# Performance work log

Measured on AMD Instinct MI355X. Metric: run time of the kernel, lower is better.

## Reference

```python
import jax, jax.numpy as jnp
import numpy as np

N_HEAD = 8
LN_EPS = 1e-5


def _ln(x, g, b):
    m = jnp.mean(x, axis=-1, keepdims=True)
    v = jnp.mean((x - m) ** 2, axis=-1, keepdims=True)
    return (x - m) * jax.lax.rsqrt(v + LN_EPS) * g + b


def setup_inputs() -> dict:
    B, S, IN, D, F, OUT, L = 4, 2048, 3, 512, 2048, 20, 6
    key = jax.random.key(0)
    ks = jax.random.split(key, 22)
    sc = 0.02
    return {
        'src': jax.random.normal(ks[0], (B, S, IN), jnp.float32),
        'W_in': jax.random.normal(ks[1], (IN, D), jnp.float32) * sc,
        'b_in': jnp.zeros((D,), jnp.float32),
        'Wq': jax.random.normal(ks[2], (L, D, D), jnp.float32) * sc,
        'bq': jnp.zeros((L, D), jnp.float32),
        'Wk': jax.random.normal(ks[3], (L, D, D), jnp.float32) * sc,
        'bk': jnp.zeros((L, D), jnp.float32),
        'Wv': jax.random.normal(ks[4], (L, D, D), jnp.float32) * sc,
        'bv': jnp.zeros((L, D), jnp.float32),
        'Wo': jax.random.normal(ks[5], (L, D, D), jnp.float32) * sc,
        'bo': jnp.zeros((L, D), jnp.float32),
        'ln1_g': jnp.ones((L, D), jnp.float32),
        'ln1_b': jnp.zeros((L, D), jnp.float32),
        'W1': jax.random.normal(ks[6], (L, D, F), jnp.float32) * sc,
        'b1': jnp.zeros((L, F), jnp.float32),
        'W2': jax.random.normal(ks[7], (L, F, D), jnp.float32) * sc,
        'b2': jnp.zeros((L, D), jnp.float32),
        'ln2_g': jnp.ones((L, D), jnp.float32),
        'ln2_b': jnp.zeros((L, D), jnp.float32),
        'W_out': jax.random.normal(ks[8], (D, OUT), jnp.float32) * sc,
        'b_out': jnp.zeros((OUT,), jnp.float32),
    }


def reference(src, W_in, b_in, Wq, bq, Wk, bk, Wv, bv, Wo, bo, ln1_g, ln1_b,
              W1, b1, W2, b2, ln2_g, ln2_b, W_out, b_out):
    x = src @ W_in + b_in            # [B, S, D]
    B, S, D = x.shape
    dh = D // N_HEAD
    scale = 1.0 / np.sqrt(dh).astype(np.float32)

    def layer(x, p):
        wq, biq, wk, bik, wv, biv, wo, bio, g1, be1, w1, bi1, w2, bi2, g2, be2 = p
        q = (x @ wq + biq).reshape(B, S, N_HEAD, dh)
        k = (x @ wk + bik).reshape(B, S, N_HEAD, dh)
        v = (x @ wv + biv).reshape(B, S, N_HEAD, dh)
        # flex_attention with score_mod=None == plain scaled dot-product attention
        scores = jnp.einsum('bqhd,bkhd->bhqk', q, k) * scale
        a = jax.nn.softmax(scores, axis=-1)
        o = jnp.einsum('bhqk,bkhd->bqhd', a, v).reshape(B, S, D)
        attn = o @ wo + bio
        h = _ln(x + attn, g1, be1)                       # post-norm (norm_first=False)
        ff = jax.nn.relu(h @ w1 + bi1) @ w2 + bi2
        h = _ln(h + ff, g2, be2)
        return h, None

    x, _ = jax.lax.scan(layer, x, (Wq, bq, Wk, bk, Wv, bv, Wo, bo,
                                   ln1_g, ln1_b, W1, b1, W2, b2, ln2_g, ln2_b))
    return x @ W_out + b_out         # [B, S, OUT]
```

## Files before the change

kernel.cpp:

```cpp
#include <hip/hip_runtime.h>

typedef unsigned short u16;
typedef unsigned int u32;
typedef __bf16 bf16x8 __attribute__((ext_vector_type(8)));
typedef float f32x4 __attribute__((ext_vector_type(4)));
typedef float f32x16 __attribute__((ext_vector_type(16)));

__device__ __forceinline__ u16 f2bf(float f) {
    union { float f; u32 u; } v; v.f = f;
    u32 r = v.u + 0x7FFFu + ((v.u >> 16) & 1u);
    return (u16)(r >> 16);
}

__device__ __forceinline__ u16 bfu(float x) {
    __bf16 b = (__bf16)x;
    union { __bf16 b; u16 u; } c; c.b = b; return c.u;
}

__device__ __forceinline__ void gload16(const u16* g, u16* l) {
    __builtin_amdgcn_global_load_lds((const __attribute__((address_space(1))) void*)g,
                                     (__attribute__((address_space(3))) void*)l, 16, 0, 0);
}

__global__ void wtrans(const float* __restrict__ W, u16* __restrict__ Wt,
                       int K, int N, int rowOff, int dstLd, long long dstStride)
{
    __shared__ float tile[32][33];
    const int l = blockIdx.z;
    const float* Wl = W + (size_t)l * K * N;
    u16* Wtl = Wt + (size_t)l * dstStride;
    const int tx = threadIdx.x, ty = threadIdx.y;
    const int x = blockIdx.x * 32 + tx;
    const int y0 = blockIdx.y * 32;
#pragma unroll
    for (int j = 0; j < 32; j += 8) tile[ty + j][tx] = Wl[(size_t)(y0 + ty + j) * N + x];
    __syncthreads();
    const int n0 = blockIdx.x * 32;
    const int k = y0 + tx;
#pragma unroll
    for (int j = 0; j < 32; j += 8)
        Wtl[(size_t)(rowOff + n0 + ty + j) * dstLd + k] = f2bf(tile[tx][ty + j]);
}

__global__ __launch_bounds__(256) void input_proj(const float* __restrict__ src,
    const float* __restrict__ Wi, const float* __restrict__ bi,
    float* __restrict__ xf, u16* __restrict__ xb)
{
    int idx = blockIdx.x * 256 + threadIdx.x;
    int m = idx >> 9, n = idx & 511;
    float v = bi[n] + src[m * 3] * Wi[n] + src[m * 3 + 1] * Wi[512 + n] + src[m * 3 + 2] * Wi[1024 + n];
    xf[idx] = v;
    xb[idx] = f2bf(v);
}

template<int EPI>
__global__ __launch_bounds__(256) void gemm_bt(
    const u16* __restrict__ A, const u16* __restrict__ Bt,
    const float* __restrict__ bias,
    float* __restrict__ Cf, u16* __restrict__ Cb,
    u16* __restrict__ Qo, u16* __restrict__ Ko, u16* __restrict__ Vo,
    const float* __restrict__ bq, const float* __restrict__ bk, const float* __restrict__ bv,
    int M, int N, int K)
{
    __shared__ u16 As[128 * 64];
    __shared__ u16 Bs[128 * 64];
    const int tid = threadIdx.x;
    const int lane = tid & 63, wid = tid >> 6;
    const int row0 = blockIdx.y * 128, col0 = blockIdx.x * 128;
    const int wr = (wid >> 1) * 64, wc = (wid & 1) * 64;
    const int cc = lane & 15, qg = lane >> 4;
    const int sr = tid >> 3, sg = tid & 7;
    f32x4 acc[4][4] = {};
    for (int k0 = 0; k0 < K; k0 += 64) {
        __syncthreads();
#pragma unroll
        for (int j = 0; j < 4; j++) {
            int r = j * 32 + sr;
            int gsw = (sg ^ (r & 7)) * 8;
            gload16(A + (size_t)(row0 + r) * K + k0 + gsw, &As[(j * 256 + tid) * 8]);
        }
#pragma unroll
        for (int j = 0; j < 4; j++) {
            int r = j * 32 + sr;
            int gsw = (sg ^ (r & 7)) * 8;
            gload16(Bt + (size_t)(col0 + r) * K + k0 + gsw, &Bs[(j * 256 + tid) * 8]);
        }
        __syncthreads();
        bf16x8 af[4][2], bfr[4][2];
#pragma unroll
        for (int i = 0; i < 4; i++) {
            int r = wr + i * 16 + cc;
#pragma unroll
            for (int kk = 0; kk < 2; kk++)
                af[i][kk] = *(const bf16x8*)&As[r * 64 + ((kk * 4 + qg) ^ (r & 7)) * 8];
        }
#pragma unroll
        for (int i = 0; i < 4; i++) {
            int r = wc + i * 16 + cc;
#pragma unroll
            for (int kk = 0; kk < 2; kk++)
                bfr[i][kk] = *(const bf16x8*)&Bs[r * 64 + ((kk * 4 + qg) ^ (r & 7)) * 8];
        }
#pragma unroll
        for (int mi = 0; mi < 4; mi++)
#pragma unroll
            for (int ni = 0; ni < 4; ni++) {
                acc[mi][ni] = __builtin_amdgcn_mfma_f32_16x16x32_bf16(af[mi][0], bfr[ni][0], acc[mi][ni], 0, 0, 0);
                acc[mi][ni] = __builtin_amdgcn_mfma_f32_16x16x32_bf16(af[mi][1], bfr[ni][1], acc[mi][ni], 0, 0, 0);
            }
    }
    const int q4 = qg * 4;
    if (EPI == 2) {
#pragma unroll
        for (int mi = 0; mi < 4; mi++) {
            int grow = row0 + wr + mi * 16 + q4;
            int btok = grow >> 11, srem = grow & 2047;
#pragma unroll
            for (int ni = 0; ni < 4; ni++) {
                int gcol = col0 + wc + ni * 16 + cc;
                int sec = gcol >> 9, f = gcol & 511;
                int hh = f >> 6, dd = f & 63;
                if (sec == 0) {
                    float bb = bq[f];
                    size_t base = (((size_t)btok * 8 + hh) * 2048 + srem) * 64 + dd;
#pragma unroll
                    for (int i = 0; i < 4; i++) Qo[base + (size_t)i * 64] = f2bf((acc[mi][ni][i] + bb) * 0.18033688f);
                } else if (sec == 1) {
                    float bb = bk[f];
                    size_t base = (((size_t)btok * 8 + hh) * 2048 + srem) * 64 + dd;
#pragma unroll
                    for (int i = 0; i < 4; i++) Ko[base + (size_t)i * 64] = f2bf(acc[mi][ni][i] + bb);
                } else {
                    float bb = bv[f];
                    size_t base = (((size_t)btok * 8 + hh) * 64 + dd) * 2048 + srem;
#pragma unroll
                    for (int i = 0; i < 4; i++) Vo[base + i] = f2bf(acc[mi][ni][i] + bb);
                }
            }
        }
    } else {
#pragma unroll
        for (int mi = 0; mi < 4; mi++) {
            int grow = row0 + wr + mi * 16 + q4;
#pragma unroll
            for (int ni = 0; ni < 4; ni++) {
                int gcol = col0 + wc + ni * 16 + cc;
                float bb = bias[gcol];
#pragma unroll
                for (int i = 0; i < 4; i++) {
                    float v = acc[mi][ni][i] + bb;
                    if (EPI == 0) Cf[(size_t)(grow + i) * N + gcol] = v;
                    else          Cb[(size_t)(grow + i) * N + gcol] = f2bf(v > 0.f ? v : 0.f);
                }
            }
        }
    }
}

__global__ __launch_bounds__(256) void gemm_bt_n64(
    const u16* __restrict__ A, const u16* __restrict__ Bt,
    const float* __restrict__ bias, float* __restrict__ Cf,
    int M, int N, int K)
{
    __shared__ u16 As[128 * 64];
    __shared__ u16 Bs[64 * 64];
    const int tid = threadIdx.x;
    const int lane = tid & 63, wid = tid >> 6;
    const int row0 = blockIdx.y * 128, col0 = blockIdx.x * 64;
    const int wr = (wid >> 1) * 64, wc = (wid & 1) * 32;
    const int cc = lane & 15, qg = lane >> 4;
    f32x4 acc[4][2] = {};
    for (int k0 = 0; k0 < K; k0 += 64) {
        __syncthreads();
#pragma unroll
        for (int j = 0; j < 4; j++) {
            int s = j * 256 + tid;
            int r = s >> 3, g = s & 7;
            gload16(A + (size_t)(row0 + r) * K + k0 + (g ^ (r & 7)) * 8, &As[s * 8]);
        }
#pragma unroll
        for (int j = 0; j < 2; j++) {
            int s = j * 256 + tid;
            int r = s >> 3, g = s & 7;
            gload16(Bt + (size_t)(col0 + r) * K + k0 + (g ^ (r & 7)) * 8, &Bs[s * 8]);
        }
        __syncthreads();
        bf16x8 af[4][2], bfr[2][2];
#pragma unroll
        for (int i = 0; i < 4; i++) {
            int r = wr + i * 16 + cc;
#pragma unroll
            for (int kk = 0; kk < 2; kk++) {
                int g = kk * 4 + qg;
                af[i][kk] = *(const bf16x8*)&As[r * 64 + (g ^ (r & 7)) * 8];
            }
        }
#pragma unroll
        for (int i = 0; i < 2; i++) {
            int r = wc + i * 16 + cc;
#pragma unroll
            for (int kk = 0; kk < 2; kk++) {
                int g = kk * 4 + qg;
                bfr[i][kk] = *(const bf16x8*)&Bs[r * 64 + (g ^ (r & 7)) * 8];
            }
        }
#pragma unroll
        for (int mi = 0; mi < 4; mi++)
#pragma unroll
            for (int ni = 0; ni < 2; ni++) {
                acc[mi][ni] = __builtin_amdgcn_mfma_f32_16x16x32_bf16(af[mi][0], bfr[ni][0], acc[mi][ni], 0, 0, 0);
                acc[mi][ni] = __builtin_amdgcn_mfma_f32_16x16x32_bf16(af[mi][1], bfr[ni][1], acc[mi][ni], 0, 0, 0);
            }
    }
    const int q4 = qg * 4;
#pragma unroll
    for (int mi = 0; mi < 4; mi++) {
        int grow = row0 + wr + mi * 16 + q4;
#pragma unroll
        for (int ni = 0; ni < 2; ni++) {
            int gcol = col0 + wc + ni * 16 + cc;
            float bb = bias[gcol];
#pragma unroll
            for (int i = 0; i < 4; i++)
                Cf[(size_t)(grow + i) * N + gcol] = acc[mi][ni][i] + bb;
        }
    }
}

__global__ __launch_bounds__(256) void flash_attn(
    const u16* __restrict__ Qb, const u16* __restrict__ Kb, const u16* __restrict__ Vt,
    u16* __restrict__ Ob)
{
    __shared__ u16 Ks[2][4096];
    __shared__ u16 Vs[2][4096];
    const int tid = threadIdx.x, lane = tid & 63, w = tid >> 6;
    const int l31 = lane & 31, h = lane >> 5;
    const int bh = blockIdx.x, qt = blockIdx.y;
    const u16* Kg = Kb + (size_t)bh * (2048 * 64);
    const u16* Vg = Vt + (size_t)bh * (64 * 2048);

    bf16x8 qf[4];
    {
        const u16* Qrow = Qb + ((size_t)bh * 2048 + (size_t)qt * 128 + w * 32 + l31) * 64;
#pragma unroll
        for (int f = 0; f < 4; f++) qf[f] = *(const bf16x8*)(Qrow + f * 16 + h * 8);
    }
    f32x16 os0{}, os1{};
    float lsum = 0.f;

    const int r8 = lane >> 3;
    const int cswz = ((lane & 7) ^ r8) * 8;
#pragma unroll
    for (int cc = 0; cc < 2; cc++) {
        int c = w * 2 + cc;
        gload16(Kg + (size_t)(c * 8 + r8) * 64 + cswz, &Ks[0][c * 512]);
        gload16(Vg + (size_t)(c * 8 + r8) * 2048 + cswz, &Vs[0][c * 512]);
    }
    const int swz = (l31 & 7) << 3;

    for (int kt = 0; kt < 32; kt++) {
        const int cur = kt & 1;
        asm volatile("s_waitcnt vmcnt(0)" ::: "memory");
        __syncthreads();
        if (kt < 31) {
#pragma unroll
            for (int cc = 0; cc < 2; cc++) {
                int c = w * 2 + cc;
                gload16(Kg + (size_t)(kt + 1) * 4096 + (size_t)(c * 8 + r8) * 64 + cswz, &Ks[cur ^ 1][c * 512]);
                gload16(Vg + (size_t)(c * 8 + r8) * 2048 + (size_t)(kt + 1) * 64 + cswz, &Vs[cur ^ 1][c * 512]);
            }
        }
        f32x16 p0{}, p1{};
        {
            const u16* kb = &Ks[cur][0];
            __builtin_amdgcn_s_setprio(1);
#pragma unroll
            for (int f = 0; f < 4; f++) {
                int colu = (f * 16 + h * 8) ^ swz;
                bf16x8 ka0 = *(const bf16x8*)(kb + l31 * 64 + colu);
                bf16x8 ka1 = *(const bf16x8*)(kb + (32 + l31) * 64 + colu);
                p0 = __builtin_amdgcn_mfma_f32_32x32x16_bf16(ka0, qf[f], p0, 0, 0, 0);
                p1 = __builtin_amdgcn_mfma_f32_32x32x16_bf16(ka1, qf[f], p1, 0, 0, 0);
            }
            __builtin_amdgcn_s_setprio(0);
        }
        float ss[4] = {};
#pragma unroll
        for (int r = 0; r < 16; r++) { float e = __builtin_amdgcn_exp2f(p0[r]); p0[r] = e; ss[r & 3] += e; }
#pragma unroll
        for (int r = 0; r < 16; r++) { float e = __builtin_amdgcn_exp2f(p1[r]); p1[r] = e; ss[r & 3] += e; }
        lsum += (ss[0] + ss[1]) + (ss[2] + ss[3]);
        const u16* vb = &Vs[cur][0];
#pragma unroll
        for (int t = 0; t < 2; t++) {
            u32 pk[8], sw[8];
#pragma unroll
            for (int j = 0; j < 8; j++) {
                float a = t ? p1[2 * j] : p0[2 * j];
                float b = t ? p1[2 * j + 1] : p0[2 * j + 1];
                pk[j] = (u32)bfu(a) | ((u32)bfu(b) << 16);
                sw[j] = __shfl_xor(pk[j], 32);
            }
            union { u32 u[4]; bf16x8 v; } fA, fB;
            fA.u[0] = h ? sw[2] : pk[0];
            fA.u[1] = h ? sw[3] : pk[1];
            fA.u[2] = h ? pk[2] : sw[0];
            fA.u[3] = h ? pk[3] : sw[1];
            fB.u[0] = h ? sw[6] : pk[4];
            fB.u[1] = h ? sw[7] : pk[5];
            fB.u[2] = h ? pk[6] : sw[4];
            fB.u[3] = h ? pk[7] : sw[5];
            __builtin_amdgcn_s_setprio(1);
#pragma unroll
            for (int f = 0; f < 2; f++) {
                bf16x8 pa = f ? fB.v : fA.v;
                int colu = (t * 32 + f * 16 + h * 8) ^ swz;
                bf16x8 v0 = *(const bf16x8*)(vb + l31 * 64 + colu);
                bf16x8 v1 = *(const bf16x8*)(vb + (32 + l31) * 64 + colu);
                os0 = __builtin_amdgcn_mfma_f32_32x32x16_bf16(pa, v0, os0, 0, 0, 0);
                os1 = __builtin_amdgcn_mfma_f32_32x32x16_bf16(pa, v1, os1, 0, 0, 0);
            }
            __builtin_amdgcn_s_setprio(0);
        }
    }
    lsum += __shfl_xor(lsum, 32);
    float rl = 1.f / lsum;
    const int hatt = bh & 7, b_ = bh >> 3;
#pragma unroll
    for (int r = 0; r < 16; r++) {
        int qrow = (r & 3) + 8 * (r >> 2) + 4 * h;
        float rlq = __shfl(rl, qrow);
        int tok = qt * 128 + w * 32 + qrow;
        u16* po = Ob + ((size_t)b_ * 2048 + tok) * 512 + hatt * 64;
        po[l31] = bfu(os0[r] * rlq);
        po[32 + l31] = bfu(os1[r] * rlq);
    }
}

__global__ __launch_bounds__(256) void ln_res(
    const float* __restrict__ X, const float* __restrict__ Y,
    const float* __restrict__ g, const float* __restrict__ bta,
    float* __restrict__ Of, u16* __restrict__ Ob)
{
    const int lane = threadIdx.x & 63;
    const int row = blockIdx.x * 4 + (threadIdx.x >> 6);
    const size_t base = (size_t)row * 512 + lane * 8;
    float4 x0 = *(const float4*)(X + base);
    float4 x1 = *(const float4*)(X + base + 4);
    float4 y0 = *(const float4*)(Y + base);
    float4 y1 = *(const float4*)(Y + base + 4);
    float t[8] = {x0.x + y0.x, x0.y + y0.y, x0.z + y0.z, x0.w + y0.w,
                  x1.x + y1.x, x1.y + y1.y, x1.z + y1.z, x1.w + y1.w};
    float s = 0.f, s2 = 0.f;
#pragma unroll
    for (int j = 0; j < 8; j++) { s += t[j]; s2 += t[j] * t[j]; }
#pragma unroll
    for (int off = 1; off < 64; off <<= 1) { s += __shfl_xor(s, off); s2 += __shfl_xor(s2, off); }
    float mean = s * (1.f / 512.f);
    float var = s2 * (1.f / 512.f) - mean * mean;
    float rs = rsqrtf(var + 1e-5f);
    float4 g0 = *(const float4*)(g + lane * 8);
    float4 g1 = *(const float4*)(g + lane * 8 + 4);
    float4 b0 = *(const float4*)(bta + lane * 8);
    float4 b1 = *(const float4*)(bta + lane * 8 + 4);
    float gg[8] = {g0.x, g0.y, g0.z, g0.w, g1.x, g1.y, g1.z, g1.w};
    float bb[8] = {b0.x, b0.y, b0.z, b0.w, b1.x, b1.y, b1.z, b1.w};
    float o[8];
#pragma unroll
    for (int j = 0; j < 8; j++) o[j] = (t[j] - mean) * rs * gg[j] + bb[j];
    *(float4*)(Of + base) = make_float4(o[0], o[1], o[2], o[3]);
    *(float4*)(Of + base + 4) = make_float4(o[4], o[5], o[6], o[7]);
    u32 p0 = (u32)f2bf(o[0]) | ((u32)f2bf(o[1]) << 16);
    u32 p1 = (u32)f2bf(o[2]) | ((u32)f2bf(o[3]) << 16);
    u32 p2 = (u32)f2bf(o[4]) | ((u32)f2bf(o[5]) << 16);
    u32 p3 = (u32)f2bf(o[6]) | ((u32)f2bf(o[7]) << 16);
    *(uint4*)(Ob + base) = make_uint4(p0, p1, p2, p3);
}

__global__ __launch_bounds__(320) void out_proj(const float* __restrict__ x,
    const float* __restrict__ W, const float* __restrict__ b, float* __restrict__ out)
{
    int t = blockIdx.x * 320 + threadIdx.x;
    int m = t / 20, o = t - m * 20;
    const float* xr = x + (size_t)m * 512;
    float acc = b[o];
#pragma unroll 8
    for (int k = 0; k < 512; k++) acc = fmaf(xr[k], W[k * 20 + o], acc);
    out[(size_t)m * 20 + o] = acc;
}

extern "C" void kernel_launch(void* const* d_in, const int* in_sizes, int n_in,
                              void* d_out, int out_size, void* d_ws, size_t ws_size,
                              hipStream_t stream)
{
    const float* src  = (const float*)d_in[0];
    const float* W_in = (const float*)d_in[1];
    const float* b_in = (const float*)d_in[2];
    const float* Wq   = (const float*)d_in[3];
    const float* bq   = (const float*)d_in[4];
    const float* Wk   = (const float*)d_in[5];
    const float* bk   = (const float*)d_in[6];
    const float* Wv   = (const float*)d_in[7];
    const float* bv   = (const float*)d_in[8];
    const float* Wo   = (const float*)d_in[9];
    const float* bo   = (const float*)d_in[10];
    const float* ln1g = (const float*)d_in[11];
    const float* ln1b = (const float*)d_in[12];
    const float* W1   = (const float*)d_in[13];
    const float* b1   = (const float*)d_in[14];
    const float* W2   = (const float*)d_in[15];
    const float* b2   = (const float*)d_in[16];
    const float* ln2g = (const float*)d_in[17];
    const float* ln2b = (const float*)d_in[18];
    const float* Wout = (const float*)d_in[19];
    const float* bout = (const float*)d_in[20];

    char* ws = (char*)d_ws;
    size_t off = 0;
    auto take = [&](size_t bytes) -> void* {
        off = (off + 255) & ~(size_t)255;
        void* p = ws + off;
        off += bytes;
        return p;
    };
    const size_t TOK = 8192, D = 512;
    u16*   qkvt = (u16*)take(6ull * 1536 * 512 * 2);
    u16*   wot  = (u16*)take(6ull * 512 * 512 * 2);
    u16*   w1t  = (u16*)take(6ull * 2048 * 512 * 2);
    u16*   w2t  = (u16*)take(6ull * 512 * 2048 * 2);
    float* xf   = (float*)take(TOK * D * 4);
    u16*   xb   = (u16*)take(TOK * D * 2);
    u16*   sh4  = (u16*)take(4ull * TOK * D * 2);
    float* scr  = (float*)take(TOK * D * 4);
    float* h1f  = (float*)take(TOK * D * 4);
    u16*   h1b  = (u16*)take(TOK * D * 2);
    if (off > ws_size) return;

    u16* qb  = sh4;
    u16* kb_ = sh4 + TOK * D;
    u16* vtb = sh4 + 2 * TOK * D;
    u16* ob  = sh4 + 3 * TOK * D;
    u16* ffb = sh4;

    dim3 tb(32, 8);
    wtrans<<<dim3(16, 16, 6), tb, 0, stream>>>(Wq, qkvt, 512, 512, 0,    512, 1536ll * 512);
    wtrans<<<dim3(16, 16, 6), tb, 0, stream>>>(Wk, qkvt, 512, 512, 512,  512, 1536ll * 512);
    wtrans<<<dim3(16, 16, 6), tb, 0, stream>>>(Wv, qkvt, 512, 512, 1024, 512, 1536ll * 512);
    wtrans<<<dim3(16, 16, 6), tb, 0, stream>>>(Wo, wot,  512, 512, 0,    512, 512ll * 512);
    wtrans<<<dim3(64, 16, 6), tb, 0, stream>>>(W1, w1t,  512, 2048, 0,   512, 2048ll * 512);
    wtrans<<<dim3(16, 64, 6), tb, 0, stream>>>(W2, w2t,  2048, 512, 0,  2048, 512ll * 2048);

    input_proj<<<16384, 256, 0, stream>>>(src, W_in, b_in, xf, xb);

    for (int l = 0; l < 6; l++) {
        const u16* qkvt_l = qkvt + (size_t)l * 1536 * 512;
        const u16* wot_l  = wot  + (size_t)l * 512 * 512;
        const u16* w1t_l  = w1t  + (size_t)l * 2048 * 512;
        const u16* w2t_l  = w2t  + (size_t)l * 512 * 2048;

        gemm_bt<2><<<dim3(12, 64), 256, 0, stream>>>(xb, qkvt_l, nullptr,
            nullptr, nullptr, qb, kb_, vtb,
            bq + l * 512, bk + l * 512, bv + l * 512, 8192, 1536, 512);

        flash_attn<<<dim3(32, 16), 256, 0, stream>>>(qb, kb_, vtb, ob);

        gemm_bt_n64<<<dim3(8, 64), 256, 0, stream>>>(ob, wot_l, bo + l * 512,
            scr, 8192, 512, 512);

        ln_res<<<2048, 256, 0, stream>>>(xf, scr, ln1g + l * 512, ln1b + l * 512, h1f, h1b);

        gemm_bt<1><<<dim3(16, 64), 256, 0, stream>>>(h1b, w1t_l, b1 + l * 2048,
            nullptr, ffb, nullptr, nullptr, nullptr, nullptr, nullptr, nullptr,
            8192, 2048, 512);

        gemm_bt_n64<<<dim3(8, 64), 256, 0, stream>>>(ffb, w2t_l, b2 + l * 512,
            scr, 8192, 512, 2048);

        ln_res<<<2048, 256, 0, stream>>>(h1f, scr, ln2g + l * 512, ln2b + l * 512, xf, xb);
    }

    out_proj<<<512, 320, 0, stream>>>(xf, Wout, bout, (float*)d_out);
}
```

Measured before the change: 1.140 ms.

## Split attention KV range across two blocks and combine partial outputs

Attention now runs with a third grid dimension that splits the 32 key tiles into two halves. Each block writes unnormalized fp32 partial outputs and row sums, and a new combine kernel adds the halves, normalizes and converts to bf16. The aim is to double the block count so the 256 CUs have more waves for latency hiding. In exchange it writes and reads large fp32 partial buffers every layer and adds an extra kernel launch. The combine simply adds the partials, which assumes both halves share the same softmax reference max.

```diff
diff --git a/kernel.cpp b/kernel.cpp
--- a/kernel.cpp
+++ b/kernel.cpp
@@ -229,13 +229,14 @@
 
 __global__ __launch_bounds__(256) void flash_attn(
     const u16* __restrict__ Qb, const u16* __restrict__ Kb, const u16* __restrict__ Vt,
-    u16* __restrict__ Ob)
+    float* __restrict__ Opart, float* __restrict__ Ls)
 {
     __shared__ u16 Ks[2][4096];
     __shared__ u16 Vs[2][4096];
     const int tid = threadIdx.x, lane = tid & 63, w = tid >> 6;
     const int l31 = lane & 31, h = lane >> 5;
-    const int bh = blockIdx.x, qt = blockIdx.y;
+    const int bh = blockIdx.x, qt = blockIdx.y, sp = blockIdx.z;
+    const int t0 = sp * 16;
     const u16* Kg = Kb + (size_t)bh * (2048 * 64);
     const u16* Vg = Vt + (size_t)bh * (64 * 2048);
 
@@ -253,21 +254,22 @@
 #pragma unroll
     for (int cc = 0; cc < 2; cc++) {
         int c = w * 2 + cc;
-        gload16(Kg + (size_t)(c * 8 + r8) * 64 + cswz, &Ks[0][c * 512]);
-        gload16(Vg + (size_t)(c * 8 + r8) * 2048 + cswz, &Vs[0][c * 512]);
+        gload16(Kg + (size_t)t0 * 4096 + (size_t)(c * 8 + r8) * 64 + cswz, &Ks[0][c * 512]);
+        gload16(Vg + (size_t)(c * 8 + r8) * 2048 + (size_t)t0 * 64 + cswz, &Vs[0][c * 512]);
     }
     const int swz = (l31 & 7) << 3;
 
-    for (int kt = 0; kt < 32; kt++) {
+    for (int kt = 0; kt < 16; kt++) {
         const int cur = kt & 1;
         asm volatile("s_waitcnt vmcnt(0)" ::: "memory");
         __syncthreads();
-        if (kt < 31) {
+        if (kt < 15) {
+            int nt = t0 + kt + 1;
 #pragma unroll
             for (int cc = 0; cc < 2; cc++) {
                 int c = w * 2 + cc;
-                gload16(Kg + (size_t)(kt + 1) * 4096 + (size_t)(c * 8 + r8) * 64 + cswz, &Ks[cur ^ 1][c * 512]);
-                gload16(Vg + (size_t)(c * 8 + r8) * 2048 + (size_t)(kt + 1) * 64 + cswz, &Vs[cur ^ 1][c * 512]);
+                gload16(Kg + (size_t)nt * 4096 + (size_t)(c * 8 + r8) * 64 + cswz, &Ks[cur ^ 1][c * 512]);
+                gload16(Vg + (size_t)(c * 8 + r8) * 2048 + (size_t)nt * 64 + cswz, &Vs[cur ^ 1][c * 512]);
             }
         }
         f32x16 p0{}, p1{};
@@ -324,17 +326,42 @@
         }
     }
     lsum += __shfl_xor(lsum, 32);
-    float rl = 1.f / lsum;
     const int hatt = bh & 7, b_ = bh >> 3;
+    if (h == 0)
+        Ls[((size_t)sp * 32 + bh) * 2048 + qt * 128 + w * 32 + l31] = lsum;
 #pragma unroll
     for (int r = 0; r < 16; r++) {
         int qrow = (r & 3) + 8 * (r >> 2) + 4 * h;
-        float rlq = __shfl(rl, qrow);
         int tok = qt * 128 + w * 32 + qrow;
-        u16* po = Ob + ((size_t)b_ * 2048 + tok) * 512 + hatt * 64;
-        po[l31] = bfu(os0[r] * rlq);
-        po[32 + l31] = bfu(os1[r] * rlq);
-    }
+        float* po = Opart + (((size_t)sp * 8192) + (size_t)b_ * 2048 + tok) * 512 + hatt * 64;
+        po[l31] = os0[r];
+        po[32 + l31] = os1[r];
+    }
+}
+
+__global__ __launch_bounds__(256) void attn_combine(
+    const float* __restrict__ Op, const float* __restrict__ Ls, u16* __restrict__ Ob)
+{
+    const int lane = threadIdx.x & 63;
+    const int row = blockIdx.x * 4 + (threadIdx.x >> 6);
+    const int b = row >> 11, srem = row & 2047;
+    const int h = lane >> 3;
+    const size_t lsidx = ((size_t)b * 8 + h) * 2048 + srem;
+    float l0 = Ls[lsidx];
+    float l1 = Ls[65536 + lsidx];
+    float rl = 1.f / (l0 + l1);
+    const size_t base = (size_t)row * 512 + lane * 8;
+    float4 a0 = *(const float4*)(Op + base);
+    float4 a1 = *(const float4*)(Op + base + 4);
+    float4 c0 = *(const float4*)(Op + 4194304 + base);
+    float4 c1 = *(const float4*)(Op + 4194304 + base + 4);
+    float o[8] = {(a0.x + c0.x) * rl, (a0.y + c0.y) * rl, (a0.z + c0.z) * rl, (a0.w + c0.w) * rl,
+                  (a1.x + c1.x) * rl, (a1.y + c1.y) * rl, (a1.z + c1.z) * rl, (a1.w + c1.w) * rl};
+    u32 p0 = (u32)f2bf(o[0]) | ((u32)f2bf(o[1]) << 16);
+    u32 p1 = (u32)f2bf(o[2]) | ((u32)f2bf(o[3]) << 16);
+    u32 p2 = (u32)f2bf(o[4]) | ((u32)f2bf(o[5]) << 16);
+    u32 p3 = (u32)f2bf(o[6]) | ((u32)f2bf(o[7]) << 16);
+    *(uint4*)(Ob + base) = make_uint4(p0, p1, p2, p3);
 }
 
 __global__ __launch_bounds__(256) void ln_res(
@@ -434,6 +461,8 @@
     float* scr  = (float*)take(TOK * D * 4);
     float* h1f  = (float*)take(TOK * D * 4);
     u16*   h1b  = (u16*)take(TOK * D * 2);
+    float* opart= (float*)take(2ull * TOK * D * 4);
+    float* lsums= (float*)take(2ull * 32 * 2048 * 4);
     if (off > ws_size) return;
 
     u16* qb  = sh4;
@@ -462,7 +491,8 @@
             nullptr, nullptr, qb, kb_, vtb,
             bq + l * 512, bk + l * 512, bv + l * 512, 8192, 1536, 512);
 
-        flash_attn<<<dim3(32, 16), 256, 0, stream>>>(qb, kb_, vtb, ob);
+        flash_attn<<<dim3(32, 16, 2), 256, 0, stream>>>(qb, kb_, vtb, opart, lsums);
+        attn_combine<<<2048, 256, 0, stream>>>(opart, lsums, ob);
 
         gemm_bt_n64<<<dim3(8, 64), 256, 0, stream>>>(ob, wot_l, bo + l * 512,
             scr, 8192, 512, 512);
```

Result: slower. 1.206 ms (+5.7%).
